# Performance work log

Hardware: AMD Instinct MI355X
Metric: run time of the kernel (lower is better)

Reference implementation:

```python
import jax, jax.numpy as jnp
import numpy as np

L = 3000          # nodes per modality
M = 3             # modalities
N = L * M         # total nodes
E = 200000        # edges
D = 512           # hidden_dim
S = D // 4        # shared_dim = 128
EPS = 1e-12       # F.normalize eps


def _lrelu(x):
    return jax.nn.leaky_relu(x, negative_slope=0.01)


def _l2norm(x):
    n = jnp.linalg.norm(x, axis=-1, keepdims=True)
    return x / jnp.maximum(n, EPS)


def setup_inputs() -> dict:
    key = jax.random.key(0)
    ks = jax.random.split(key, 16)
    w = lambda k, shape: (jax.random.normal(k, shape, dtype=jnp.float32) * 0.02)
    inp = {
        "feat0": jax.random.normal(ks[0], (L, D), dtype=jnp.float32),
        "feat1": jax.random.normal(ks[1], (L, D), dtype=jnp.float32),
        "feat2": jax.random.normal(ks[2], (L, D), dtype=jnp.float32),
        "edge_index": jax.random.randint(ks[3], (2, E), 0, N, dtype=jnp.int64),
        # EdgeWeightGen params (torch Linear convention: weight is (out, in))
        "proj_w": w(ks[4], (S, D)),
        "mlp_w1": w(ks[5], (S, 2 * S)),
        "mlp_b1": jnp.zeros((S,), dtype=jnp.float32),
        "mlp_w2": w(ks[6], (1, S)),
        "mlp_b2": jnp.zeros((1,), dtype=jnp.float32),
        # CrossModalGraphLayer params, 2 layers
        "W1_0": w(ks[7], (D, D)),
        "W2_0": w(ks[8], (D, 2 * D)),
        "W1_1": w(ks[9], (D, D)),
        "W2_1": w(ks[10], (D, 2 * D)),
    }
    return inp


def reference(feat0, feat1, feat2, edge_index, proj_w, mlp_w1, mlp_b1,
              mlp_w2, mlp_b2, W1_0, W2_0, W1_1, W2_1):
    feature = jnp.concatenate([feat0, feat1, feat2], axis=0)  # (N, D)
    src, tgt = edge_index[0], edge_index[1]

    # EdgeWeightGen
    shared_src = _l2norm(feature[src] @ proj_w.T)   # (E, S)
    shared_tgt = _l2norm(feature[tgt] @ proj_w.T)   # (E, S)
    emb_cat = jnp.concatenate([shared_src, shared_tgt], axis=-1)  # (E, 2S)
    h = _lrelu(emb_cat @ mlp_w1.T + mlp_b1)
    edge_weight = jax.nn.sigmoid((h @ mlp_w2.T + mlp_b2)[:, 0])   # (E,)

    # build_adj_matrix: dense scatter-add (sparse_coo coalesce sums dups)
    adj = jnp.zeros((N, N), dtype=feature.dtype).at[src, tgt].add(edge_weight)
    row_sum = adj.sum(axis=1)
    d_inv_sqrt = jnp.where(row_sum > 0, row_sum ** -0.5, 0.0)
    # D^{-1/2} A D^{-1/2} as elementwise row/col scaling (same math as diag matmuls)
    gcn = d_inv_sqrt[:, None] * adj * d_inv_sqrt[None, :]

    # graph layers
    x = feature
    for W1, W2 in ((W1_0, W2_0), (W1_1, W2_1)):
        proj = x @ W1.T                 # (N, D)
        nb = gcn @ proj                 # (N, D)
        cat = jnp.concatenate([x + nb, x * nb], axis=-1)  # (N, 2D)
        x = _lrelu(cat @ W2.T)
    return x  # concatenated updated features; chunk(x, 3) recovers per-modal tuple
```

## Files before the change

### kernel.cpp

```cpp
#include <hip/hip_runtime.h>
#include <hip/hip_bf16.h>
#include <math.h>

#define NL 3000
#define NN 9000
#define NE 200000
#define DD 512
#define SS 128
#define MPAD 9088
#define MT   (MPAD/16)

typedef __attribute__((ext_vector_type(8))) short    bf16x8;
typedef __attribute__((ext_vector_type(8))) ushort   u16x8;
typedef __attribute__((ext_vector_type(4))) float    f32x4;

static __device__ __forceinline__ float dot4(float4 a, float4 b){ return a.x*b.x+a.y*b.y+a.z*b.z+a.w*b.w; }
static __device__ __forceinline__ ushort f2bf(float f){
  unsigned u = __float_as_uint(f);
  return (ushort)((u + 0x7FFFu + ((u>>16)&1u)) >> 16);
}
static __device__ __forceinline__ float bf2f(ushort u){
  return __uint_as_float(((unsigned)u)<<16);
}

__global__ void k_concat(const float* __restrict__ f0, const float* __restrict__ f1,
                         const float* __restrict__ f2, float* __restrict__ feat){
  int i = blockIdx.x*blockDim.x+threadIdx.x;
  const int per = NL*DD/4, tot = NN*DD/4;
  if (i>=tot) return;
  const float4* s; int j=i;
  if (j<per) s=(const float4*)f0;
  else if (j<2*per){ s=(const float4*)f1; j-=per; }
  else { s=(const float4*)f2; j-=2*per; }
  ((float4*)feat)[i]=s[j];
}

__global__ __launch_bounds__(256) void k_pack(const float* __restrict__ X, short* __restrict__ P,
                                              int M, int K, int nTilesK){
  int t = blockIdx.x*4 + (threadIdx.x>>6);
  int lane = threadIdx.x & 63;
  int tm = t / nTilesK, tk = t - tm*nTilesK;
  int m = tm*16 + (lane&15);
  int k = tk*32 + (lane>>4)*8;
  float4 v0 = make_float4(0,0,0,0), v1 = make_float4(0,0,0,0);
  if (m < M){
    v0 = *(const float4*)(X + (size_t)m*K + k);
    v1 = *(const float4*)(X + (size_t)m*K + k + 4);
  }
  u16x8 r;
  r[0]=f2bf(v0.x); r[1]=f2bf(v0.y); r[2]=f2bf(v0.z); r[3]=f2bf(v0.w);
  r[4]=f2bf(v1.x); r[5]=f2bf(v1.y); r[6]=f2bf(v1.z); r[7]=f2bf(v1.w);
  *(u16x8*)(P + (size_t)t*512 + lane*8) = r;
}

__global__ __launch_bounds__(256) void k_packb(const ushort* __restrict__ X, short* __restrict__ P,
                                               int M, int K, int nTilesK){
  int t = blockIdx.x*4 + (threadIdx.x>>6);
  int lane = threadIdx.x & 63;
  int tm = t / nTilesK, tk = t - tm*nTilesK;
  int m = tm*16 + (lane&15);
  int k = tk*32 + (lane>>4)*8;
  u16x8 r = {0,0,0,0,0,0,0,0};
  if (m < M) r = *(const u16x8*)(X + (size_t)m*K + k);
  *(u16x8*)(P + (size_t)t*512 + lane*8) = r;
}

__global__ __launch_bounds__(256) void k_pack_w1(const float* __restrict__ w1, short* __restrict__ P){
  int t = blockIdx.x*4 + (threadIdx.x>>6);
  int lane = threadIdx.x & 63;
  int tn = t >> 2, tk = t & 3;
  int n = tn*16 + (lane&15);
  int k = tk*32 + (lane>>4)*8;
  const float* sp = (n<128) ? (w1 + (size_t)n*256 + k) : (w1 + (size_t)(n-128)*256 + 128 + k);
  float4 v0 = *(const float4*)sp;
  float4 v1 = *(const float4*)(sp+4);
  u16x8 r;
  r[0]=f2bf(v0.x); r[1]=f2bf(v0.y); r[2]=f2bf(v0.z); r[3]=f2bf(v0.w);
  r[4]=f2bf(v1.x); r[5]=f2bf(v1.y); r[6]=f2bf(v1.z); r[7]=f2bf(v1.w);
  *(u16x8*)(P + (size_t)t*512 + lane*8) = r;
}

__global__ __launch_bounds__(256) void k_cat_pack(const float* __restrict__ x, const float* __restrict__ nb,
                                                  short* __restrict__ P){
  const int nTilesK = 32;
  int t = blockIdx.x*4 + (threadIdx.x>>6);
  int lane = threadIdx.x & 63;
  int tm = t / nTilesK, tk = t - tm*nTilesK;
  int m = tm*16 + (lane&15);
  int k = tk*32 + (lane>>4)*8;
  int kk = k & 511;
  bool mul = (k >= 512);
  float4 x0 = make_float4(0,0,0,0), x1 = x0, n0 = x0, n1 = x0;
  if (m < NN){
    x0 = *(const float4*)(x + (size_t)m*DD + kk);
    x1 = *(const float4*)(x + (size_t)m*DD + kk + 4);
    n0 = *(const float4*)(nb + (size_t)m*DD + kk);
    n1 = *(const float4*)(nb + (size_t)m*DD + kk + 4);
  }
  float v[8];
  if (mul){
    v[0]=x0.x*n0.x; v[1]=x0.y*n0.y; v[2]=x0.z*n0.z; v[3]=x0.w*n0.w;
    v[4]=x1.x*n1.x; v[5]=x1.y*n1.y; v[6]=x1.z*n1.z; v[7]=x1.w*n1.w;
  } else {
    v[0]=x0.x+n0.x; v[1]=x0.y+n0.y; v[2]=x0.z+n0.z; v[3]=x0.w+n0.w;
    v[4]=x1.x+n1.x; v[5]=x1.y+n1.y; v[6]=x1.z+n1.z; v[7]=x1.w+n1.w;
  }
  u16x8 r;
  #pragma unroll
  for (int j=0;j<8;++j) r[j]=f2bf(v[j]);
  *(u16x8*)(P + (size_t)t*512 + lane*8) = r;
}

template<int ACT, int OBF>
__global__ __launch_bounds__(256) void k_gmm(const short* __restrict__ Ap, const short* __restrict__ Bp,
                                             void* __restrict__ Cv, int M, int N, int K){
  int lane = threadIdx.x & 63, wave = threadIdx.x >> 6;
  int ktiles = K >> 5;
  int bm = blockIdx.y*128 + wave*32;
  int bn = blockIdx.x*64;
  const bf16x8* a0 = (const bf16x8*)(Ap + ((size_t)((bm>>4)  ) * ktiles)*512 + lane*8);
  const bf16x8* a1 = (const bf16x8*)(Ap + ((size_t)((bm>>4)+1) * ktiles)*512 + lane*8);
  const bf16x8* b0 = (const bf16x8*)(Bp + ((size_t)((bn>>4)  ) * ktiles)*512 + lane*8);
  const bf16x8* b1 = (const bf16x8*)(Bp + ((size_t)((bn>>4)+1) * ktiles)*512 + lane*8);
  const bf16x8* b2 = (const bf16x8*)(Bp + ((size_t)((bn>>4)+2) * ktiles)*512 + lane*8);
  const bf16x8* b3 = (const bf16x8*)(Bp + ((size_t)((bn>>4)+3) * ktiles)*512 + lane*8);
  f32x4 acc[2][4];
  #pragma unroll
  for (int i=0;i<2;++i)
    #pragma unroll
    for (int j=0;j<4;++j) acc[i][j] = (f32x4){0.f,0.f,0.f,0.f};

  for (int kt=0; kt<ktiles; ++kt){
    int off = kt*64;
    bf16x8 A0 = a0[off], A1 = a1[off];
    bf16x8 B0 = b0[off], B1 = b1[off], B2 = b2[off], B3 = b3[off];
    acc[0][0] = __builtin_amdgcn_mfma_f32_16x16x32_bf16(A0, B0, acc[0][0], 0,0,0);
    acc[0][1] = __builtin_amdgcn_mfma_f32_16x16x32_bf16(A0, B1, acc[0][1], 0,0,0);
    acc[0][2] = __builtin_amdgcn_mfma_f32_16x16x32_bf16(A0, B2, acc[0][2], 0,0,0);
    acc[0][3] = __builtin_amdgcn_mfma_f32_16x16x32_bf16(A0, B3, acc[0][3], 0,0,0);
    acc[1][0] = __builtin_amdgcn_mfma_f32_16x16x32_bf16(A1, B0, acc[1][0], 0,0,0);
    acc[1][1] = __builtin_amdgcn_mfma_f32_16x16x32_bf16(A1, B1, acc[1][1], 0,0,0);
    acc[1][2] = __builtin_amdgcn_mfma_f32_16x16x32_bf16(A1, B2, acc[1][2], 0,0,0);
    acc[1][3] = __builtin_amdgcn_mfma_f32_16x16x32_bf16(A1, B3, acc[1][3], 0,0,0);
  }
  int colo = lane & 15;
  int rowo = (lane >> 4) * 4;
  #pragma unroll
  for (int mi=0; mi<2; ++mi){
    #pragma unroll
    for (int r=0; r<4; ++r){
      int row = bm + mi*16 + rowo + r;
      if (row < M){
        #pragma unroll
        for (int ni=0; ni<4; ++ni){
          float v = acc[mi][ni][r];
          if (ACT) v = v>0.f ? v : 0.01f*v;
          int cidx = bn + ni*16 + colo;
          if (OBF) ((ushort*)Cv)[(size_t)row*N + cidx] = f2bf(v);
          else     ((float*) Cv)[(size_t)row*N + cidx] = v;
        }
      }
    }
  }
}

__global__ __launch_bounds__(256) void k_l2n(const float* __restrict__ X, ushort* __restrict__ Y){
  int lane = threadIdx.x & 63, wave = threadIdx.x >> 6;
  int m = blockIdx.x*4 + wave;
  float2 v = ((const float2*)(X + (size_t)m*SS))[lane];
  float ss = v.x*v.x + v.y*v.y;
  #pragma unroll
  for (int o=32;o>0;o>>=1) ss += __shfl_xor(ss, o);
  float inv = 1.f / fmaxf(sqrtf(ss), 1e-12f);
  ushort2 r; r.x = f2bf(v.x*inv); r.y = f2bf(v.y*inv);
  ((ushort2*)(Y + (size_t)m*SS))[lane] = r;
}

__global__ __launch_bounds__(256) void k_edge(const int* __restrict__ src, const int* __restrict__ tgt,
                      const ushort* __restrict__ AB,
                      const float* __restrict__ b1, const float* __restrict__ w2,
                      const float* __restrict__ b2p,
                      float* __restrict__ ew, float* __restrict__ row_sum, int* __restrict__ cnt){
  int lane = threadIdx.x & 63;
  int wid = blockIdx.x*(blockDim.x>>6) + (threadIdx.x>>6);
  int nw  = gridDim.x*(blockDim.x>>6);
  float2 b1v = ((const float2*)b1)[lane];
  float2 w2v = ((const float2*)w2)[lane];
  float b2 = b2p[0];
  for (int e=wid; e<NE; e+=nw){
    int s = src[e], tg = tgt[e];
    ushort2 a2 = ((const ushort2*)(AB + (size_t)s*256))[lane];
    ushort2 c2 = ((const ushort2*)(AB + (size_t)tg*256 + 128))[lane];
    float hx = bf2f(a2.x) + bf2f(c2.x) + b1v.x;
    float hy = bf2f(a2.y) + bf2f(c2.y) + b1v.y;
    hx = hx>0.f ? hx : 0.01f*hx;
    hy = hy>0.f ? hy : 0.01f*hy;
    float p = hx*w2v.x + hy*w2v.y;
    #pragma unroll
    for (int o=32;o>0;o>>=1) p += __shfl_xor(p, o);
    if (lane==0){
      float wgt = 1.f/(1.f+expf(-(p+b2)));
      ew[e]=wgt;
      atomicAdd(&row_sum[s], wgt);
      atomicAdd(&cnt[s], 1);
    }
  }
}

__global__ __launch_bounds__(1024) void k_scan(const int* __restrict__ cnt, const float* __restrict__ row_sum,
                      int* __restrict__ row_ptr, float* __restrict__ dinv, int* __restrict__ fill){
  __shared__ int sdata[1024];
  __shared__ int carry;
  int t = threadIdx.x;
  if (t==0) carry=0;
  __syncthreads();
  for (int base=0;base<NN;base+=1024){
    int i = base+t;
    int v = (i<NN)? cnt[i] : 0;
    if (i<NN){
      float rs = row_sum[i];
      dinv[i] = rs>0.f ? (1.f/sqrtf(rs)) : 0.f;
      fill[i] = 0;
    }
    sdata[t]=v; __syncthreads();
    for (int o=1;o<1024;o<<=1){
      int x = (t>=o)? sdata[t-o] : 0;
      __syncthreads();
      sdata[t]+=x;
      __syncthreads();
    }
    if (i<NN) row_ptr[i] = carry + sdata[t]-v;
    int tot = sdata[1023];
    __syncthreads();
    if (t==0) carry += tot;
    __syncthreads();
  }
  if (t==0) row_ptr[NN] = carry;
}

__global__ __launch_bounds__(256) void k_scatter(const int* __restrict__ src, const int* __restrict__ tgt,
                        const float* __restrict__ ew, const float* __restrict__ dinv,
                        const int* __restrict__ row_ptr, int* __restrict__ fill,
                        int* __restrict__ col, float* __restrict__ coef){
  int e = blockIdx.x*blockDim.x+threadIdx.x;
  if (e>=NE) return;
  int s=src[e], tg=tgt[e];
  int pos = atomicAdd(&fill[s],1);
  int idx = row_ptr[s]+pos;
  col[idx]=tg;
  coef[idx]=dinv[s]*ew[e]*dinv[tg];
}

__global__ __launch_bounds__(128) void k_spmm_bf(const int* __restrict__ row_ptr, const int* __restrict__ col,
                     const float* __restrict__ coef, const ushort* __restrict__ proj,
                     float* __restrict__ nb){
  int m = blockIdx.x, t = threadIdx.x;
  int beg = row_ptr[m], end = row_ptr[m+1];
  float4 acc0 = make_float4(0,0,0,0), acc1 = make_float4(0,0,0,0);
  int j = beg;
  for (; j+2<=end; j+=2){
    int t0 = col[j], t1 = col[j+1];
    float c0 = coef[j], c1 = coef[j+1];
    ushort4 p0 = ((const ushort4*)(proj + (size_t)t0*DD))[t];
    ushort4 p1 = ((const ushort4*)(proj + (size_t)t1*DD))[t];
    acc0.x += c0*bf2f(p0.x); acc0.y += c0*bf2f(p0.y);
    acc0.z += c0*bf2f(p0.z); acc0.w += c0*bf2f(p0.w);
    acc1.x += c1*bf2f(p1.x); acc1.y += c1*bf2f(p1.y);
    acc1.z += c1*bf2f(p1.z); acc1.w += c1*bf2f(p1.w);
  }
  if (j < end){
    int t0 = col[j]; float c0 = coef[j];
    ushort4 p0 = ((const ushort4*)(proj + (size_t)t0*DD))[t];
    acc0.x += c0*bf2f(p0.x); acc0.y += c0*bf2f(p0.y);
    acc0.z += c0*bf2f(p0.z); acc0.w += c0*bf2f(p0.w);
  }
  acc0.x += acc1.x; acc0.y += acc1.y; acc0.z += acc1.z; acc0.w += acc1.w;
  ((float4*)(nb + (size_t)m*DD))[t] = acc0;
}

extern "C" void kernel_launch(void* const* d_in, const int* in_sizes, int n_in,
                              void* d_out, int out_size, void* d_ws, size_t ws_size,
                              hipStream_t stream){
  const float* f0 = (const float*)d_in[0];
  const float* f1 = (const float*)d_in[1];
  const float* f2 = (const float*)d_in[2];
  const int*   ei = (const int*)d_in[3];
  const float* pw = (const float*)d_in[4];
  const float* w1 = (const float*)d_in[5];
  const float* b1 = (const float*)d_in[6];
  const float* w2 = (const float*)d_in[7];
  const float* b2 = (const float*)d_in[8];
  const float* W1_0 = (const float*)d_in[9];
  const float* W2_0 = (const float*)d_in[10];
  const float* W1_1 = (const float*)d_in[11];
  const float* W2_1 = (const float*)d_in[12];
  float* out = (float*)d_out;

  const int* src = ei;
  const int* tgt = ei + NE;

  char* base = (char*)d_ws;
  size_t o = 0;
  auto alloc = [&](size_t bytes)->char*{ char* p = base + o; o += (bytes + 1023) & ~size_t(1023); return p; };
  float* feature = (float*)alloc((size_t)NN*DD*4);
  float* x1      = (float*)alloc((size_t)NN*DD*4);
  float* nb      = (float*)alloc((size_t)NN*DD*4);
  ushort* projbf = (ushort*)alloc((size_t)NN*DD*2);
  float* projS   = (float*)alloc((size_t)NN*SS*4);
  ushort* shbf   = (ushort*)alloc((size_t)NN*SS*2);
  ushort* ABn    = (ushort*)alloc((size_t)NN*256*2);
  short* Apack1  = (short*)alloc((size_t)MT*16*1024);
  short* Apack2  = (short*)alloc((size_t)MT*32*1024);
  short* ShP     = (short*)alloc((size_t)MT*4*1024);
  short* BpF     = (short*)alloc((size_t)8*16*1024);
  short* Bpab    = (short*)alloc((size_t)16*4*1024);
  short* Bp10    = (short*)alloc((size_t)32*16*1024);
  short* Bp20    = (short*)alloc((size_t)32*32*1024);
  short* Bp11    = (short*)alloc((size_t)32*16*1024);
  short* Bp21    = (short*)alloc((size_t)32*32*1024);
  float* ew      = (float*)alloc(NE*4);
  float* coef    = (float*)alloc(NE*4);
  float* row_sum = (float*)alloc(NN*4);
  int*   cnt     = (int*)alloc(NN*4);
  float* dinv    = (float*)alloc(NN*4);
  int*   fill    = (int*)alloc(NN*4);
  int*   row_ptr = (int*)alloc((NN+1)*4);
  int*   col     = (int*)alloc(NE*4);

  hipMemsetAsync(row_sum, 0, NN*4, stream);
  hipMemsetAsync(cnt, 0, NN*4, stream);

  k_concat<<<(NN*DD/4+255)/256, 256, 0, stream>>>(f0,f1,f2,feature);
  k_pack<<<MT*16/4, 256, 0, stream>>>(feature, Apack1, NN, DD, 16);

  k_pack<<<8*16/4, 256, 0, stream>>>(pw, BpF, 128, 512, 16);
  dim3 gF(128/64, MPAD/128);
  k_gmm<0,0><<<gF, 256, 0, stream>>>(Apack1, BpF, projS, NN, 128, 512);
  k_l2n<<<NN/4, 256, 0, stream>>>(projS, shbf);
  k_packb<<<MT*4/4, 256, 0, stream>>>(shbf, ShP, NN, 128, 4);
  k_pack_w1<<<16, 256, 0, stream>>>(w1, Bpab);
  dim3 gAB(256/64, MPAD/128);
  k_gmm<0,1><<<gAB, 256, 0, stream>>>(ShP, Bpab, ABn, NN, 256, 128);

  k_edge<<<4096, 256, 0, stream>>>(src,tgt,ABn,b1,w2,b2,ew,row_sum,cnt);
  k_scan<<<1, 1024, 0, stream>>>(cnt,row_sum,row_ptr,dinv,fill);
  k_scatter<<<(NE+255)/256, 256, 0, stream>>>(src,tgt,ew,dinv,row_ptr,fill,col,coef);

  k_pack<<<128, 256, 0, stream>>>(W1_0, Bp10, 512, 512, 16);
  k_pack<<<256, 256, 0, stream>>>(W2_0, Bp20, 512, 1024, 32);
  k_pack<<<128, 256, 0, stream>>>(W1_1, Bp11, 512, 512, 16);
  k_pack<<<256, 256, 0, stream>>>(W2_1, Bp21, 512, 1024, 32);

  dim3 gg(512/64, MPAD/128);
  k_gmm<0,1><<<gg, 256, 0, stream>>>(Apack1, Bp10, projbf, NN, DD, DD);
  k_spmm_bf<<<NN, 128, 0, stream>>>(row_ptr, col, coef, projbf, nb);
  k_cat_pack<<<MT*32/4, 256, 0, stream>>>(feature, nb, Apack2);
  k_gmm<1,0><<<gg, 256, 0, stream>>>(Apack2, Bp20, x1, NN, DD, 2*DD);
  k_pack<<<MT*16/4, 256, 0, stream>>>(x1, Apack1, NN, DD, 16);
  k_gmm<0,1><<<gg, 256, 0, stream>>>(Apack1, Bp11, projbf, NN, DD, DD);
  k_spmm_bf<<<NN, 128, 0, stream>>>(row_ptr, col, coef, projbf, nb);
  k_cat_pack<<<MT*32/4, 256, 0, stream>>>(x1, nb, Apack2);
  k_gmm<1,0><<<gg, 256, 0, stream>>>(Apack2, Bp21, out, NN, DD, 2*DD);
}
```

Before: 387.5 us.

## Fuse packing kernels, batch weight packing, and rework edge, scan, SpMM kernels

Merges the concat and bf16 pack into one kernel, packs all five weight matrices in a single launch, and has the L2-normalize kernel write the MFMA-packed layout directly, dropping the separate packb pass. The edge kernel now processes four edges per wave with 16 lanes each and 8-wide loads. The single-block scan is replaced by a per-thread chunked warp-shuffle scan, and the SpMM inner loop is unrolled by four with independent accumulators. Together these cut the number of launches, intermediate buffers and barrier-heavy scan steps, at the cost of more register pressure in the SpMM and edge kernels.

```diff
diff --git a/kernel.cpp b/kernel.cpp
--- a/kernel.cpp
+++ b/kernel.cpp
@@ -14,7 +14,6 @@
 typedef __attribute__((ext_vector_type(8))) ushort   u16x8;
 typedef __attribute__((ext_vector_type(4))) float    f32x4;
 
-static __device__ __forceinline__ float dot4(float4 a, float4 b){ return a.x*b.x+a.y*b.y+a.z*b.z+a.w*b.w; }
 static __device__ __forceinline__ ushort f2bf(float f){
   unsigned u = __float_as_uint(f);
   return (ushort)((u + 0x7FFFu + ((u>>16)&1u)) >> 16);
@@ -23,29 +22,23 @@
   return __uint_as_float(((unsigned)u)<<16);
 }
 
-__global__ void k_concat(const float* __restrict__ f0, const float* __restrict__ f1,
-                         const float* __restrict__ f2, float* __restrict__ feat){
-  int i = blockIdx.x*blockDim.x+threadIdx.x;
-  const int per = NL*DD/4, tot = NN*DD/4;
-  if (i>=tot) return;
-  const float4* s; int j=i;
-  if (j<per) s=(const float4*)f0;
-  else if (j<2*per){ s=(const float4*)f1; j-=per; }
-  else { s=(const float4*)f2; j-=2*per; }
-  ((float4*)feat)[i]=s[j];
-}
-
-__global__ __launch_bounds__(256) void k_pack(const float* __restrict__ X, short* __restrict__ P,
-                                              int M, int K, int nTilesK){
+__global__ __launch_bounds__(256) void k_cpack(const float* __restrict__ f0, const float* __restrict__ f1,
+                                               const float* __restrict__ f2,
+                                               float* __restrict__ feat, short* __restrict__ P){
   int t = blockIdx.x*4 + (threadIdx.x>>6);
   int lane = threadIdx.x & 63;
-  int tm = t / nTilesK, tk = t - tm*nTilesK;
+  int tm = t >> 4, tk = t & 15;
   int m = tm*16 + (lane&15);
   int k = tk*32 + (lane>>4)*8;
-  float4 v0 = make_float4(0,0,0,0), v1 = make_float4(0,0,0,0);
-  if (m < M){
-    v0 = *(const float4*)(X + (size_t)m*K + k);
-    v1 = *(const float4*)(X + (size_t)m*K + k + 4);
+  float4 v0 = make_float4(0,0,0,0), v1 = v0;
+  if (m < NN){
+    const float* srow = (m < NL) ? f0 + (size_t)m*DD
+                       : (m < 2*NL) ? f1 + (size_t)(m-NL)*DD
+                       : f2 + (size_t)(m-2*NL)*DD;
+    v0 = *(const float4*)(srow + k);
+    v1 = *(const float4*)(srow + k + 4);
+    *(float4*)(feat + (size_t)m*DD + k)     = v0;
+    *(float4*)(feat + (size_t)m*DD + k + 4) = v1;
   }
   u16x8 r;
   r[0]=f2bf(v0.x); r[1]=f2bf(v0.y); r[2]=f2bf(v0.z); r[3]=f2bf(v0.w);
@@ -53,16 +46,47 @@
   *(u16x8*)(P + (size_t)t*512 + lane*8) = r;
 }
 
-__global__ __launch_bounds__(256) void k_packb(const ushort* __restrict__ X, short* __restrict__ P,
-                                               int M, int K, int nTilesK){
+__global__ __launch_bounds__(256) void k_pack(const float* __restrict__ X, short* __restrict__ P,
+                                              int M, int K, int nTilesK){
   int t = blockIdx.x*4 + (threadIdx.x>>6);
   int lane = threadIdx.x & 63;
   int tm = t / nTilesK, tk = t - tm*nTilesK;
   int m = tm*16 + (lane&15);
   int k = tk*32 + (lane>>4)*8;
-  u16x8 r = {0,0,0,0,0,0,0,0};
-  if (m < M) r = *(const u16x8*)(X + (size_t)m*K + k);
+  float4 v0 = make_float4(0,0,0,0), v1 = v0;
+  if (m < M){
+    v0 = *(const float4*)(X + (size_t)m*K + k);
+    v1 = *(const float4*)(X + (size_t)m*K + k + 4);
+  }
+  u16x8 r;
+  r[0]=f2bf(v0.x); r[1]=f2bf(v0.y); r[2]=f2bf(v0.z); r[3]=f2bf(v0.w);
+  r[4]=f2bf(v1.x); r[5]=f2bf(v1.y); r[6]=f2bf(v1.z); r[7]=f2bf(v1.w);
   *(u16x8*)(P + (size_t)t*512 + lane*8) = r;
+}
+
+__global__ __launch_bounds__(256) void k_wpack5(const float* __restrict__ pw,
+                                                const float* __restrict__ W10, const float* __restrict__ W20,
+                                                const float* __restrict__ W11, const float* __restrict__ W21,
+                                                short* __restrict__ BpF,
+                                                short* __restrict__ Bp10, short* __restrict__ Bp20,
+                                                short* __restrict__ Bp11, short* __restrict__ Bp21){
+  int t = blockIdx.x*4 + (threadIdx.x>>6);
+  int lane = threadIdx.x & 63;
+  const float* X; short* P; int K, ntk, lt;
+  if (t < 128)      { X=pw;  P=BpF;  K=512;  ntk=16; lt=t; }
+  else if (t < 640) { X=W10; P=Bp10; K=512;  ntk=16; lt=t-128; }
+  else if (t < 1664){ X=W20; P=Bp20; K=1024; ntk=32; lt=t-640; }
+  else if (t < 2176){ X=W11; P=Bp11; K=512;  ntk=16; lt=t-1664; }
+  else              { X=W21; P=Bp21; K=1024; ntk=32; lt=t-2176; }
+  int tm = lt/ntk, tk = lt - tm*ntk;
+  int m = tm*16 + (lane&15);
+  int k = tk*32 + (lane>>4)*8;
+  float4 v0 = *(const float4*)(X + (size_t)m*K + k);
+  float4 v1 = *(const float4*)(X + (size_t)m*K + k + 4);
+  u16x8 r;
+  r[0]=f2bf(v0.x); r[1]=f2bf(v0.y); r[2]=f2bf(v0.z); r[3]=f2bf(v0.w);
+  r[4]=f2bf(v1.x); r[5]=f2bf(v1.y); r[6]=f2bf(v1.z); r[7]=f2bf(v1.w);
+  *(u16x8*)(P + (size_t)lt*512 + lane*8) = r;
 }
 
 __global__ __launch_bounds__(256) void k_pack_w1(const float* __restrict__ w1, short* __restrict__ P){
@@ -164,7 +188,7 @@
   }
 }
 
-__global__ __launch_bounds__(256) void k_l2n(const float* __restrict__ X, ushort* __restrict__ Y){
+__global__ __launch_bounds__(256) void k_l2n(const float* __restrict__ X, short* __restrict__ ShP){
   int lane = threadIdx.x & 63, wave = threadIdx.x >> 6;
   int m = blockIdx.x*4 + wave;
   float2 v = ((const float2*)(X + (size_t)m*SS))[lane];
@@ -172,8 +196,11 @@
   #pragma unroll
   for (int o=32;o>0;o>>=1) ss += __shfl_xor(ss, o);
   float inv = 1.f / fmaxf(sqrtf(ss), 1e-12f);
+  int k = 2*lane;
+  int tIdx = (m>>4)*4 + (k>>5);
+  int pos  = ((m&15) + ((k>>3)&3)*16)*8 + (k&7);
   ushort2 r; r.x = f2bf(v.x*inv); r.y = f2bf(v.y*inv);
-  ((ushort2*)(Y + (size_t)m*SS))[lane] = r;
+  *(ushort2*)(ShP + (size_t)tIdx*512 + pos) = r;
 }
 
 __global__ __launch_bounds__(256) void k_edge(const int* __restrict__ src, const int* __restrict__ tgt,
@@ -182,24 +209,29 @@
                       const float* __restrict__ b2p,
                       float* __restrict__ ew, float* __restrict__ row_sum, int* __restrict__ cnt){
   int lane = threadIdx.x & 63;
+  int p = lane & 15, g = lane >> 4;
   int wid = blockIdx.x*(blockDim.x>>6) + (threadIdx.x>>6);
   int nw  = gridDim.x*(blockDim.x>>6);
-  float2 b1v = ((const float2*)b1)[lane];
-  float2 w2v = ((const float2*)w2)[lane];
+  float4 b1a = ((const float4*)b1)[p*2], b1b = ((const float4*)b1)[p*2+1];
+  float4 w2a = ((const float4*)w2)[p*2], w2b = ((const float4*)w2)[p*2+1];
+  float bb[8] = {b1a.x,b1a.y,b1a.z,b1a.w,b1b.x,b1b.y,b1b.z,b1b.w};
+  float ww[8] = {w2a.x,w2a.y,w2a.z,w2a.w,w2b.x,w2b.y,w2b.z,w2b.w};
   float b2 = b2p[0];
-  for (int e=wid; e<NE; e+=nw){
-    int s = src[e], tg = tgt[e];
-    ushort2 a2 = ((const ushort2*)(AB + (size_t)s*256))[lane];
-    ushort2 c2 = ((const ushort2*)(AB + (size_t)tg*256 + 128))[lane];
-    float hx = bf2f(a2.x) + bf2f(c2.x) + b1v.x;
-    float hy = bf2f(a2.y) + bf2f(c2.y) + b1v.y;
-    hx = hx>0.f ? hx : 0.01f*hx;
-    hy = hy>0.f ? hy : 0.01f*hy;
-    float p = hx*w2v.x + hy*w2v.y;
+  for (int e = wid*4+g; e < NE; e += nw*4){
+    int s = src[e], tg_ = tgt[e];
+    u16x8 av = *(const u16x8*)(AB + (size_t)s*256 + p*8);
+    u16x8 bv = *(const u16x8*)(AB + (size_t)tg_*256 + 128 + p*8);
+    float acc = 0.f;
     #pragma unroll
-    for (int o=32;o>0;o>>=1) p += __shfl_xor(p, o);
-    if (lane==0){
-      float wgt = 1.f/(1.f+expf(-(p+b2)));
+    for (int i=0;i<8;++i){
+      float h = bf2f(av[i]) + bf2f(bv[i]) + bb[i];
+      h = h>0.f ? h : 0.01f*h;
+      acc += h*ww[i];
+    }
+    acc += __shfl_xor(acc,1); acc += __shfl_xor(acc,2);
+    acc += __shfl_xor(acc,4); acc += __shfl_xor(acc,8);
+    if (p==0){
+      float wgt = 1.f/(1.f+expf(-(acc+b2)));
       ew[e]=wgt;
       atomicAdd(&row_sum[s], wgt);
       atomicAdd(&cnt[s], 1);
@@ -209,33 +241,49 @@
 
 __global__ __launch_bounds__(1024) void k_scan(const int* __restrict__ cnt, const float* __restrict__ row_sum,
                       int* __restrict__ row_ptr, float* __restrict__ dinv, int* __restrict__ fill){
-  __shared__ int sdata[1024];
-  __shared__ int carry;
+  __shared__ int wsum[16];
   int t = threadIdx.x;
-  if (t==0) carry=0;
+  int lane = t & 63, wid = t >> 6;
+  const int CH = 9;
+  int base = t*CH;
+  int v[CH]; int s = 0;
+  #pragma unroll
+  for (int i=0;i<CH;++i){
+    int idx = base+i;
+    v[i] = (idx<NN) ? cnt[idx] : 0;
+    s += v[i];
+  }
+  int ps = s;
+  #pragma unroll
+  for (int o=1;o<64;o<<=1){
+    int x = __shfl_up(ps, o);
+    if (lane >= o) ps += x;
+  }
+  if (lane==63) wsum[wid] = ps;
   __syncthreads();
-  for (int base=0;base<NN;base+=1024){
-    int i = base+t;
-    int v = (i<NN)? cnt[i] : 0;
-    if (i<NN){
-      float rs = row_sum[i];
-      dinv[i] = rs>0.f ? (1.f/sqrtf(rs)) : 0.f;
-      fill[i] = 0;
+  if (wid==0){
+    int wv = (lane<16)? wsum[lane] : 0;
+    #pragma unroll
+    for (int o=1;o<16;o<<=1){
+      int x = __shfl_up(wv, o);
+      if (lane>=o) wv += x;
     }
-    sdata[t]=v; __syncthreads();
-    for (int o=1;o<1024;o<<=1){
-      int x = (t>=o)? sdata[t-o] : 0;
-      __syncthreads();
-      sdata[t]+=x;
-      __syncthreads();
+    if (lane<16) wsum[lane]=wv;
+  }
+  __syncthreads();
+  int prefix = (wid>0 ? wsum[wid-1] : 0) + (ps - s);
+  #pragma unroll
+  for (int i=0;i<CH;++i){
+    int idx = base+i;
+    if (idx<NN){
+      row_ptr[idx] = prefix;
+      float rs = row_sum[idx];
+      dinv[idx] = rs>0.f ? (1.f/sqrtf(rs)) : 0.f;
+      fill[idx] = 0;
+      prefix += v[i];
     }
-    if (i<NN) row_ptr[i] = carry + sdata[t]-v;
-    int tot = sdata[1023];
-    __syncthreads();
-    if (t==0) carry += tot;
-    __syncthreads();
-  }
-  if (t==0) row_ptr[NN] = carry;
+  }
+  if (t==1023) row_ptr[NN] = wsum[15];
 }
 
 __global__ __launch_bounds__(256) void k_scatter(const int* __restrict__ src, const int* __restrict__ tgt,
@@ -256,26 +304,30 @@
                      float* __restrict__ nb){
   int m = blockIdx.x, t = threadIdx.x;
   int beg = row_ptr[m], end = row_ptr[m+1];
-  float4 acc0 = make_float4(0,0,0,0), acc1 = make_float4(0,0,0,0);
+  float4 a0 = make_float4(0,0,0,0), a1 = a0, a2 = a0, a3 = a0;
   int j = beg;
-  for (; j+2<=end; j+=2){
-    int t0 = col[j], t1 = col[j+1];
-    float c0 = coef[j], c1 = coef[j+1];
-    ushort4 p0 = ((const ushort4*)(proj + (size_t)t0*DD))[t];
-    ushort4 p1 = ((const ushort4*)(proj + (size_t)t1*DD))[t];
-    acc0.x += c0*bf2f(p0.x); acc0.y += c0*bf2f(p0.y);
-    acc0.z += c0*bf2f(p0.z); acc0.w += c0*bf2f(p0.w);
-    acc1.x += c1*bf2f(p1.x); acc1.y += c1*bf2f(p1.y);
-    acc1.z += c1*bf2f(p1.z); acc1.w += c1*bf2f(p1.w);
-  }
-  if (j < end){
-    int t0 = col[j]; float c0 = coef[j];
-    ushort4 p0 = ((const ushort4*)(proj + (size_t)t0*DD))[t];
-    acc0.x += c0*bf2f(p0.x); acc0.y += c0*bf2f(p0.y);
-    acc0.z += c0*bf2f(p0.z); acc0.w += c0*bf2f(p0.w);
-  }
-  acc0.x += acc1.x; acc0.y += acc1.y; acc0.z += acc1.z; acc0.w += acc1.w;
-  ((float4*)(nb + (size_t)m*DD))[t] = acc0;
+  for (; j+4<=end; j+=4){
+    int c0=col[j], c1=col[j+1], c2=col[j+2], c3=col[j+3];
+    float w0=coef[j], w1=coef[j+1], w2_=coef[j+2], w3=coef[j+3];
+    ushort4 p0 = ((const ushort4*)(proj + (size_t)c0*DD))[t];
+    ushort4 p1 = ((const ushort4*)(proj + (size_t)c1*DD))[t];
+    ushort4 p2 = ((const ushort4*)(proj + (size_t)c2*DD))[t];
+    ushort4 p3 = ((const ushort4*)(proj + (size_t)c3*DD))[t];
+    a0.x += w0*bf2f(p0.x); a0.y += w0*bf2f(p0.y); a0.z += w0*bf2f(p0.z); a0.w += w0*bf2f(p0.w);
+    a1.x += w1*bf2f(p1.x); a1.y += w1*bf2f(p1.y); a1.z += w1*bf2f(p1.z); a1.w += w1*bf2f(p1.w);
+    a2.x += w2_*bf2f(p2.x); a2.y += w2_*bf2f(p2.y); a2.z += w2_*bf2f(p2.z); a2.w += w2_*bf2f(p2.w);
+    a3.x += w3*bf2f(p3.x); a3.y += w3*bf2f(p3.y); a3.z += w3*bf2f(p3.z); a3.w += w3*bf2f(p3.w);
+  }
+  for (; j<end; ++j){
+    int c0=col[j]; float w0=coef[j];
+    ushort4 p0 = ((const ushort4*)(proj + (size_t)c0*DD))[t];
+    a0.x += w0*bf2f(p0.x); a0.y += w0*bf2f(p0.y); a0.z += w0*bf2f(p0.z); a0.w += w0*bf2f(p0.w);
+  }
+  a0.x += a1.x + a2.x + a3.x;
+  a0.y += a1.y + a2.y + a3.y;
+  a0.z += a1.z + a2.z + a3.z;
+  a0.w += a1.w + a2.w + a3.w;
+  ((float4*)(nb + (size_t)m*DD))[t] = a0;
 }
 
 extern "C" void kernel_launch(void* const* d_in, const int* in_sizes, int n_in,
@@ -307,7 +359,6 @@
   float* nb      = (float*)alloc((size_t)NN*DD*4);
   ushort* projbf = (ushort*)alloc((size_t)NN*DD*2);
   float* projS   = (float*)alloc((size_t)NN*SS*4);
-  ushort* shbf   = (ushort*)alloc((size_t)NN*SS*2);
   ushort* ABn    = (ushort*)alloc((size_t)NN*256*2);
   short* Apack1  = (short*)alloc((size_t)MT*16*1024);
   short* Apack2  = (short*)alloc((size_t)MT*32*1024);
@@ -330,26 +381,19 @@
   hipMemsetAsync(row_sum, 0, NN*4, stream);
   hipMemsetAsync(cnt, 0, NN*4, stream);
 
-  k_concat<<<(NN*DD/4+255)/256, 256, 0, stream>>>(f0,f1,f2,feature);
-  k_pack<<<MT*16/4, 256, 0, stream>>>(feature, Apack1, NN, DD, 16);
-
-  k_pack<<<8*16/4, 256, 0, stream>>>(pw, BpF, 128, 512, 16);
+  k_cpack<<<MT*16/4, 256, 0, stream>>>(f0,f1,f2,feature,Apack1);
+  k_wpack5<<<800, 256, 0, stream>>>(pw,W1_0,W2_0,W1_1,W2_1,BpF,Bp10,Bp20,Bp11,Bp21);
+  k_pack_w1<<<16, 256, 0, stream>>>(w1, Bpab);
+
   dim3 gF(128/64, MPAD/128);
   k_gmm<0,0><<<gF, 256, 0, stream>>>(Apack1, BpF, projS, NN, 128, 512);
-  k_l2n<<<NN/4, 256, 0, stream>>>(projS, shbf);
-  k_packb<<<MT*4/4, 256, 0, stream>>>(shbf, ShP, NN, 128, 4);
-  k_pack_w1<<<16, 256, 0, stream>>>(w1, Bpab);
+  k_l2n<<<NN/4, 256, 0, stream>>>(projS, ShP);
   dim3 gAB(256/64, MPAD/128);
   k_gmm<0,1><<<gAB, 256, 0, stream>>>(ShP, Bpab, ABn, NN, 256, 128);
 
-  k_edge<<<4096, 256, 0, stream>>>(src,tgt,ABn,b1,w2,b2,ew,row_sum,cnt);
+  k_edge<<<2048, 256, 0, stream>>>(src,tgt,ABn,b1,w2,b2,ew,row_sum,cnt);
   k_scan<<<1, 1024, 0, stream>>>(cnt,row_sum,row_ptr,dinv,fill);
   k_scatter<<<(NE+255)/256, 256, 0, stream>>>(src,tgt,ew,dinv,row_ptr,fill,col,coef);
-
-  k_pack<<<128, 256, 0, stream>>>(W1_0, Bp10, 512, 512, 16);
-  k_pack<<<256, 256, 0, stream>>>(W2_0, Bp20, 512, 1024, 32);
-  k_pack<<<128, 256, 0, stream>>>(W1_1, Bp11, 512, 512, 16);
-  k_pack<<<256, 256, 0, stream>>>(W2_1, Bp21, 512, 1024, 32);
 
   dim3 gg(512/64, MPAD/128);
   k_gmm<0,1><<<gg, 256, 0, stream>>>(Apack1, Bp10, projbf, NN, DD, DD);
```

Measured after the change: 359.7 us. -7.2%, faster.
